# Kernel tuning notes

Measured on AMD Instinct MI355X. Metric: run time of the kernel, lower is better.

## Reference

```python
import jax, jax.numpy as jnp
import numpy as np

DIM = 256
HEADS = 8
HEAD_DIM = 32
INNER = HEADS * HEAD_DIM  # 256
B, L_AG, H, W = 2, 5, 32, 32
SEQ = H * W
POS_HID = 32


def _lin(k, fan_in, fan_out):
    kw, kb = jax.random.split(k)
    Wt = jax.random.normal(kw, (fan_in, fan_out), jnp.float32) * (fan_in ** -0.5)
    b = jax.random.normal(kb, (fan_out,), jnp.float32) * 0.01
    return Wt, b


def setup_inputs() -> dict:
    key = jax.random.key(0)
    ks = jax.random.split(key, 10)
    x = jax.random.normal(ks[0], (B, L_AG, H, W, DIM), jnp.float32)
    Wq, bq = _lin(ks[1], DIM, INNER)
    Wk, bk = _lin(ks[2], DIM, INNER)
    Wv, bv = _lin(ks[3], DIM, INNER)
    Wp1, bp1 = _lin(ks[4], 3, POS_HID)
    Wp2, bp2 = _lin(ks[5], POS_HID, HEADS)
    Ws1, bs1 = _lin(ks[6], DIM, POS_HID)
    Ws2, bs2 = _lin(ks[7], POS_HID, HEADS)
    Wo, bo = _lin(ks[8], INNER, DIM)
    Wg, bg = _lin(ks[9], 2 * DIM, DIM)
    return dict(x=x, Wq=Wq, bq=bq, Wk=Wk, bk=bk, Wv=Wv, bv=bv,
                Wp1=Wp1, bp1=bp1, Wp2=Wp2, bp2=bp2,
                Ws1=Ws1, bs1=bs1, Ws2=Ws2, bs2=bs2,
                Wo=Wo, bo=bo, Wg=Wg, bg=bg)


def _relative_positions(h, w):
    # coords: (h*w, 2), row-major (i//w, i%w) like torch meshgrid 'ij'
    yy, xx = jnp.meshgrid(jnp.arange(h), jnp.arange(w), indexing='ij')
    coords = jnp.stack([yy.reshape(-1), xx.reshape(-1)], axis=-1)  # (L,2)
    rel = (coords[:, None, :] - coords[None, :, :]).astype(jnp.float32)  # (L,L,2)
    dist = jnp.linalg.norm(rel, axis=-1, keepdims=True)  # (L,L,1)
    return jnp.concatenate([rel, dist], axis=-1)  # (L,L,3)


def reference(x, Wq, bq, Wk, bk, Wv, bv, Wp1, bp1, Wp2, bp2,
              Ws1, bs1, Ws2, bs2, Wo, bo, Wg, bg):
    b, l, h, w, c = x.shape
    bl, L = b * l, h * w
    scale = HEAD_DIM ** -0.5
    x2 = x.reshape(bl, L, c)

    q = (x2 @ Wq + bq).reshape(bl, L, HEADS, HEAD_DIM)
    k = (x2 @ Wk + bk).reshape(bl, L, HEADS, HEAD_DIM)
    v = (x2 @ Wv + bv).reshape(bl, L, HEADS, HEAD_DIM)

    scores = jnp.einsum('bihd,bjhd->bhij', q, k) * scale  # (bl,H,L,L)

    rel_pos = _relative_positions(h, w)  # (L,L,3)
    pos_w = jax.nn.relu(rel_pos @ Wp1 + bp1) @ Wp2 + bp2  # (L,L,heads)
    pos_w = jnp.transpose(pos_w, (2, 0, 1))[None]  # (1,heads,L,L)

    s = jax.nn.relu(x2 @ Ws1 + bs1) @ Ws2 + bs2  # (bl,L,heads)
    fsim = jnp.einsum('bih,bjh->bij', s, s)[:, None]  # (bl,1,L,L)

    probs = jax.nn.softmax(scores + pos_w + fsim, axis=-1)
    out = jnp.einsum('bhij,bjhd->bihd', probs, v).reshape(bl, L, INNER)
    out = out @ Wo + bo  # (bl,L,dim); dropout is identity in eval

    gate = jax.nn.sigmoid(jnp.concatenate([x2, out], axis=-1) @ Wg + bg)
    out = gate * out + (1.0 - gate) * x2
    return out.reshape(b, l, h, w, c)
```

## Files before the change

### kernel.cpp

```cpp
#include <hip/hip_runtime.h>

typedef __bf16 bf16_t;
typedef __bf16 bf16x4 __attribute__((ext_vector_type(4)));
typedef __bf16 bf16x8 __attribute__((ext_vector_type(8)));
typedef float  f32x4  __attribute__((ext_vector_type(4)));

#define HEADS 8
#define HEAD_DIM 32
#define DIM 256
#define BL 10
#define SEQ 1024
#define M_TOTAL (BL*SEQ)
#define QK_SCALE 0.17677669529663687f
#define LOG2E 1.4426950408889634f
#define SQRT_LOG2E 1.2011224087864498f
#define NPOS (63*63)

#define NCAST 2596
#define NTRANS 96
#define NPREP (NCAST + NTRANS + 16)

__device__ __forceinline__ int swz_idx(int row, int col) {
  return row*64 + (col ^ ((row & 7) << 3));
}
__device__ __forceinline__ int swz256(int row, int col) {
  return row*256 + (col ^ ((row & 7) << 3));
}

__global__ __launch_bounds__(256) void prep_all_kernel(
    const float* __restrict__ x, const float* __restrict__ Ws1,
    const float* __restrict__ bq, const float* __restrict__ bk,
    const float* __restrict__ bv, const float* __restrict__ bs1,
    const float* __restrict__ Wq, const float* __restrict__ Wk, const float* __restrict__ Wv,
    const float* __restrict__ Wo, const float* __restrict__ Wg,
    const float* __restrict__ Wp1, const float* __restrict__ bp1,
    const float* __restrict__ Wp2, const float* __restrict__ bp2,
    bf16_t* __restrict__ xb, bf16_t* __restrict__ btall, float* __restrict__ bias_all,
    bf16_t* __restrict__ wot, bf16_t* __restrict__ wg1t, bf16_t* __restrict__ wg2t,
    float* __restrict__ posT)
{
  __shared__ float tile[64][65];
  const int bid = blockIdx.x;
  const int tid = threadIdx.x;

  if (bid < NCAST) {
    const int NX4 = M_TOTAL*DIM/4;
    const int i = bid*256 + tid;
    if (i < NX4) {
      const float4 v = ((const float4*)x)[i];
      bf16x4 o; o[0]=(bf16_t)v.x; o[1]=(bf16_t)v.y; o[2]=(bf16_t)v.z; o[3]=(bf16_t)v.w;
      *(bf16x4*)(xb + (size_t)i*4) = o;
      return;
    }
    int idx = i - NX4;
    if (idx < 8192) {
      const int m = idx >> 8, k = idx & 255;
      btall[(768 + m)*256 + k] = (bf16_t)Ws1[k*32 + m];
      return;
    }
    idx -= 8192;
    if (idx < 832) {
      bias_all[idx] = (idx < 256) ? bq[idx] : (idx < 512) ? bk[idx-256] :
                      (idx < 768) ? bv[idx-512] : (idx < 800) ? bs1[idx-768] : 0.f;
    }
    return;
  }

  if (bid < NCAST + NTRANS) {
    const int t0 = bid - NCAST;
    const int z = t0 >> 4, bi = (t0 & 15) >> 2, bj = t0 & 3;
    const float* src; bf16_t* dst;
    switch (z) {
      case 0: src = Wq;          dst = btall;          break;
      case 1: src = Wk;          dst = btall + 65536;  break;
      case 2: src = Wv;          dst = btall + 131072; break;
      case 3: src = Wo;          dst = wot;            break;
      case 4: src = Wg;          dst = wg1t;           break;
      default: src = Wg + 65536; dst = wg2t;           break;
    }
    const int tr = tid >> 4, tc = tid & 15;
    #pragma unroll
    for (int i = 0; i < 4; ++i) {
      const float4 v = *(const float4*)(src + (size_t)(bi*64 + tr + 16*i)*256 + bj*64 + tc*4);
      float* tp = &tile[tr + 16*i][tc*4];
      tp[0]=v.x; tp[1]=v.y; tp[2]=v.z; tp[3]=v.w;
    }
    __syncthreads();
    #pragma unroll
    for (int i = 0; i < 4; ++i) {
      bf16x4 o;
      #pragma unroll
      for (int e = 0; e < 4; ++e) o[e] = (bf16_t)tile[tc*4 + e][tr + 16*i];
      *(bf16x4*)(dst + (size_t)(bj*64 + tr + 16*i)*256 + bi*64 + tc*4) = o;
    }
    return;
  }

  {
    float* sm = &tile[0][0];
    float* w1 = sm; float* b1 = sm + 96; float* w2 = sm + 128; float* b2 = sm + 384;
    if (tid < 96) w1[tid] = Wp1[tid];
    if (tid < 32) b1[tid] = bp1[tid];
    w2[tid] = Wp2[tid];
    if (tid < 8)  b2[tid] = bp2[tid];
    __syncthreads();
    const int p = (bid - NCAST - NTRANS)*256 + tid;
    if (p >= NPOS) return;
    const float dy = (float)(p / 63 - 31);
    const float dx = (float)(p % 63 - 31);
    const float dist = sqrtf(dy*dy + dx*dx);
    float o[8];
    #pragma unroll
    for (int t = 0; t < 8; ++t) o[t] = b2[t];
    #pragma unroll
    for (int m = 0; m < 32; ++m) {
      float hv = fmaf(dy, w1[m], fmaf(dx, w1[32+m], fmaf(dist, w1[64+m], b1[m])));
      hv = fmaxf(hv, 0.f);
      #pragma unroll
      for (int t = 0; t < 8; ++t) o[t] = fmaf(hv, w2[m*8+t], o[t]);
    }
    #pragma unroll
    for (int t = 0; t < 8; ++t) posT[t*NPOS + p] = o[t]*LOG2E;
  }
}

__global__ __launch_bounds__(256) void qkv_kernel(
    const bf16_t* __restrict__ xb, const bf16_t* __restrict__ btall,
    const float* __restrict__ bias_all, const float* __restrict__ Ws2,
    const float* __restrict__ bs2,
    bf16_t* __restrict__ qbuf, bf16_t* __restrict__ kbuf, bf16_t* __restrict__ vbuf,
    bf16_t* __restrict__ sbb)
{
  __shared__ float hidlds[64][33];
  const int mt = blockIdx.x, ngb = blockIdx.y;
  const int tid = threadIdx.x;
  const int w = tid >> 6, lane = tid & 63, g = lane >> 4, l15 = lane & 15;
  const int arow = mt*64 + w*16 + l15;
  const bf16x8* Arow = (const bf16x8*)(xb + (size_t)arow*DIM);
  bf16x8 af[8];
  #pragma unroll
  for (int kc = 0; kc < 8; ++kc) af[kc] = Arow[kc*4 + g];
  if (ngb < 12) {
    bf16_t* dst = (ngb < 4) ? qbuf : (ngb < 8) ? kbuf : vbuf;
    const int coloff = (ngb & 3) * 64;
    const float scale = (ngb < 4) ? QK_SCALE*LOG2E : 1.f;
    for (int c = 0; c < 4; ++c) {
      const int n = ngb*64 + c*16 + l15;
      const bf16x8* Brow = (const bf16x8*)(btall + (size_t)n*DIM);
      f32x4 acc = {0.f,0.f,0.f,0.f};
      #pragma unroll
      for (int kc = 0; kc < 8; ++kc)
        acc = __builtin_amdgcn_mfma_f32_16x16x32_bf16(af[kc], Brow[kc*4+g], acc, 0, 0, 0);
      const float bvv = bias_all[n];
      #pragma unroll
      for (int r = 0; r < 4; ++r) {
        const int row = mt*64 + w*16 + g*4 + r;
        dst[(size_t)row*DIM + coloff + c*16 + l15] = (bf16_t)((acc[r] + bvv)*scale);
      }
    }
  } else {
    for (int c = 0; c < 2; ++c) {
      const int n = 768 + c*16 + l15;
      const bf16x8* Brow = (const bf16x8*)(btall + (size_t)n*DIM);
      f32x4 acc = {0.f,0.f,0.f,0.f};
      #pragma unroll
      for (int kc = 0; kc < 8; ++kc)
        acc = __builtin_amdgcn_mfma_f32_16x16x32_bf16(af[kc], Brow[kc*4+g], acc, 0, 0, 0);
      const float bvv = bias_all[n];
      #pragma unroll
      for (int r = 0; r < 4; ++r)
        hidlds[w*16 + g*4 + r][c*16 + l15] = fmaxf(acc[r] + bvv, 0.f);
    }
    __syncthreads();
    if (tid < 64) {
      float sv[8];
      #pragma unroll
      for (int t = 0; t < 8; ++t) sv[t] = bs2[t];
      #pragma unroll
      for (int m = 0; m < 32; ++m) {
        const float hv = hidlds[tid][m];
        #pragma unroll
        for (int t = 0; t < 8; ++t) sv[t] = fmaf(hv, Ws2[m*8+t], sv[t]);
      }
      bf16x8 o;
      #pragma unroll
      for (int t = 0; t < 8; ++t) o[t] = (bf16_t)(sv[t]*SQRT_LOG2E);
      *(bf16x8*)(sbb + (size_t)(mt*64 + tid)*8) = o;
    }
  }
}

__global__ __launch_bounds__(256) void attn_kernel(
    const bf16_t* __restrict__ qb, const bf16_t* __restrict__ kb,
    const bf16_t* __restrict__ vb, const bf16_t* __restrict__ sbb,
    const float* __restrict__ posT, bf16_t* __restrict__ att)
{
  __shared__ __align__(16) bf16_t lk[64*64];
  __shared__ __align__(16) bf16_t lv[48*64];
  __shared__ __align__(16) bf16_t lp[64*64];
  __shared__ float ptab[33*63];

  const int wg = blockIdx.x;
  const int xcd = wg & 7, within = wg >> 3;
  const int pair = xcd*10 + (within >> 4);
  const int it = within & 15;
  const int h = pair & 7, b = pair >> 3;
  const int i0 = it*64, iy0 = it*2;
  const int tid = threadIdx.x;
  const int w = tid >> 6, lane = tid & 63, g = lane >> 4, l15 = lane & 15;
  const int r4 = tid >> 2, q4 = tid & 3;

  for (int p = tid; p < 33*63; p += 256) {
    const int rr = p / 63, cc = p - rr*63;
    ptab[p] = posT[h*NPOS + (iy0 + rr)*63 + cc];
  }
  for (int p = tid; p < 16*64; p += 256) {
    const int d = 32 + (p >> 6), j = p & 63;
    lv[d*64 + (j ^ ((d & 7) << 3))] = (bf16_t)((d == 32) ? 1.f : 0.f);
  }
  for (int p = tid; p < 192; p += 256) {
    const int rr = p / 3, ch = 5 + (p % 3);
    bf16x8 z = {};
    *(bf16x8*)&lk[swz_idx(rr, ch*8)] = z;
  }

  const int qrow = b*SEQ + i0 + w*16 + l15;
  const bf16x8 aq0 = *(const bf16x8*)(qb + (size_t)qrow*DIM + h*HEAD_DIM + g*8);
  bf16x8 aq1 = {};
  if (g == 0) aq1 = *(const bf16x8*)(sbb + (size_t)qrow*8);

  const int iq = i0 + w*16 + l15;
  const int rbase_i = (iq >> 5) - iy0 + 31;
  const int ixr = iq & 31;

  bf16x8 kreg = *(const bf16x8*)(kb + (size_t)(b*SEQ + r4)*DIM + h*HEAD_DIM + q4*8);
  bf16x8 vreg = *(const bf16x8*)(vb + (size_t)(b*SEQ + r4)*DIM + h*HEAD_DIM + q4*8);
  bf16x8 sreg = {};
  if (tid < 64) sreg = *(const bf16x8*)(sbb + (size_t)(b*SEQ + tid)*8);

  f32x4 accO0 = {0.f,0.f,0.f,0.f}, accO1 = {0.f,0.f,0.f,0.f}, accO2 = {0.f,0.f,0.f,0.f};
  float mrow = -1e30f;

  for (int jt = 0; jt < 16; ++jt) {
    const int j0 = jt*64;
    __syncthreads();
    *(bf16x8*)&lk[swz_idx(r4, q4*8)] = kreg;
    #pragma unroll
    for (int e = 0; e < 8; ++e) {
      const int d = q4*8 + e;
      lv[d*64 + (r4 ^ ((d & 7) << 3))] = vreg[e];
    }
    if (tid < 64) *(bf16x8*)&lk[swz_idx(tid, 32)] = sreg;
    __syncthreads();

    if (jt < 15) {
      const int grow = b*SEQ + j0 + 64;
      kreg = *(const bf16x8*)(kb + (size_t)(grow + r4)*DIM + h*HEAD_DIM + q4*8);
      vreg = *(const bf16x8*)(vb + (size_t)(grow + r4)*DIM + h*HEAD_DIM + q4*8);
      if (tid < 64) sreg = *(const bf16x8*)(sbb + (size_t)(grow + tid)*8);
    }

    f32x4 s4[4];
    #pragma unroll
    for (int c = 0; c < 4; ++c) {
      const bf16x8 kf0 = *(const bf16x8*)&lk[swz_idx(c*16 + l15, g*8)];
      const bf16x8 kf1 = *(const bf16x8*)&lk[swz_idx(c*16 + l15, 32 + g*8)];
      f32x4 acc = {0.f,0.f,0.f,0.f};
      acc = __builtin_amdgcn_mfma_f32_16x16x32_bf16(kf0, aq0, acc, 0, 0, 0);
      acc = __builtin_amdgcn_mfma_f32_16x16x32_bf16(kf1, aq1, acc, 0, 0, 0);
      s4[c] = acc;
    }

    #pragma unroll
    for (int c = 0; c < 4; ++c) {
      #pragma unroll
      for (int r = 0; r < 4; ++r) {
        const int jl = c*16 + g*4 + r;
        const int jy = jt*2 + (jl >> 5);
        const int jx = jl & 31;
        s4[c][r] += ptab[(rbase_i - jy)*63 + (ixr - jx + 31)];
      }
    }

    float m16 = s4[0][0];
    #pragma unroll
    for (int c = 0; c < 4; ++c) {
      #pragma unroll
      for (int r = 0; r < 4; ++r) m16 = fmaxf(m16, s4[c][r]);
    }
    m16 = fmaxf(m16, __shfl_xor(m16, 16));
    m16 = fmaxf(m16, __shfl_xor(m16, 32));
    if (__any(m16 > mrow + 8.f)) {
      const float mn = fmaxf(mrow, m16);
      const float alpha = exp2f(mrow - mn);
      mrow = mn;
      #pragma unroll
      for (int r = 0; r < 4; ++r) {
        const float aO = __shfl(alpha, g*16 + g*4 + r);
        accO0[r] *= aO; accO1[r] *= aO; accO2[r] *= aO;
      }
    }
    #pragma unroll
    for (int c = 0; c < 4; ++c) {
      #pragma unroll
      for (int r = 0; r < 4; ++r) s4[c][r] = exp2f(s4[c][r] - mrow);
    }

    #pragma unroll
    for (int c = 0; c < 4; ++c) {
      bf16x4 o;
      #pragma unroll
      for (int r = 0; r < 4; ++r) o[r] = (bf16_t)s4[c][r];
      *(bf16x4*)&lp[swz_idx(w*16 + l15, c*16 + g*4)] = o;
    }

    const int prow = w*16 + l15;
    #pragma unroll
    for (int kc = 0; kc < 2; ++kc) {
      const bf16x8 ap  = *(const bf16x8*)&lp[swz_idx(prow, kc*32 + g*8)];
      const bf16x8 bv0 = *(const bf16x8*)&lv[swz_idx(l15,      kc*32 + g*8)];
      const bf16x8 bv1 = *(const bf16x8*)&lv[swz_idx(16 + l15, kc*32 + g*8)];
      const bf16x8 bv2 = *(const bf16x8*)&lv[swz_idx(32 + l15, kc*32 + g*8)];
      accO0 = __builtin_amdgcn_mfma_f32_16x16x32_bf16(ap, bv0, accO0, 0, 0, 0);
      accO1 = __builtin_amdgcn_mfma_f32_16x16x32_bf16(ap, bv1, accO1, 0, 0, 0);
      accO2 = __builtin_amdgcn_mfma_f32_16x16x32_bf16(ap, bv2, accO2, 0, 0, 0);
    }
  }

  #pragma unroll
  for (int r = 0; r < 4; ++r) {
    const int row = b*SEQ + i0 + w*16 + g*4 + r;
    const float lsum = __shfl(accO2[r], lane & 48);
    const float inv = 1.f / lsum;
    att[(size_t)row*DIM + h*HEAD_DIM + l15]      = (bf16_t)(accO0[r]*inv);
    att[(size_t)row*DIM + h*HEAD_DIM + 16 + l15] = (bf16_t)(accO1[r]*inv);
  }
}

__global__ __launch_bounds__(256) void prjgate_kernel(
    const bf16_t* __restrict__ att, const bf16_t* __restrict__ wot,
    const float* __restrict__ bo, const bf16_t* __restrict__ xb,
    const float* __restrict__ x, const bf16_t* __restrict__ wg1t,
    const bf16_t* __restrict__ wg2t, const float* __restrict__ bg,
    float* __restrict__ outp)
{
  __shared__ __align__(16) bf16_t prjT[16*256];
  const int row0 = blockIdx.x * 16;
  const int tid = threadIdx.x;
  const int w = tid >> 6, lane = tid & 63, g = lane >> 4, l15 = lane & 15;
  const int arow = row0 + l15;

  {
    const bf16x8* Arow = (const bf16x8*)(att + (size_t)arow*DIM);
    bf16x8 afA[8];
    #pragma unroll
    for (int kc = 0; kc < 8; ++kc) afA[kc] = Arow[kc*4 + g];
    #pragma unroll
    for (int ct = 0; ct < 4; ++ct) {
      const int n = w*64 + ct*16 + l15;
      const bf16x8* Brow = (const bf16x8*)(wot + (size_t)n*DIM);
      f32x4 acc = {0.f,0.f,0.f,0.f};
      #pragma unroll
      for (int kc = 0; kc < 8; ++kc)
        acc = __builtin_amdgcn_mfma_f32_16x16x32_bf16(afA[kc], Brow[kc*4+g], acc, 0, 0, 0);
      const float bvo = bo[n];
      #pragma unroll
      for (int r = 0; r < 4; ++r)
        prjT[swz256(g*4 + r, n)] = (bf16_t)(acc[r] + bvo);
    }
  }
  __syncthreads();

  const bf16x8* A1r = (const bf16x8*)(xb + (size_t)arow*DIM);
  bf16x8 a1[8], a2[8];
  #pragma unroll
  for (int kc = 0; kc < 8; ++kc) {
    a1[kc] = A1r[kc*4 + g];
    a2[kc] = *(const bf16x8*)&prjT[swz256(l15, kc*32 + g*8)];
  }
  #pragma unroll
  for (int ct = 0; ct < 4; ++ct) {
    const int n = w*64 + ct*16 + l15;
    const bf16x8* b1 = (const bf16x8*)(wg1t + (size_t)n*DIM);
    const bf16x8* b2 = (const bf16x8*)(wg2t + (size_t)n*DIM);
    f32x4 acc = {0.f,0.f,0.f,0.f};
    #pragma unroll
    for (int kc = 0; kc < 8; ++kc)
      acc = __builtin_amdgcn_mfma_f32_16x16x32_bf16(a1[kc], b1[kc*4+g], acc, 0, 0, 0);
    #pragma unroll
    for (int kc = 0; kc < 8; ++kc)
      acc = __builtin_amdgcn_mfma_f32_16x16x32_bf16(a2[kc], b2[kc*4+g], acc, 0, 0, 0);
    const float bgv = bg[n];
    #pragma unroll
    for (int r = 0; r < 4; ++r) {
      const int grow = row0 + g*4 + r;
      const float gate = 1.f / (1.f + __expf(-(acc[r] + bgv)));
      const float pv = (float)prjT[swz256(g*4 + r, n)];
      const float xv = x[(size_t)grow*DIM + n];
      outp[(size_t)grow*DIM + n] = gate*pv + (1.f - gate)*xv;
    }
  }
}

extern "C" void kernel_launch(void* const* d_in, const int* in_sizes, int n_in,
                              void* d_out, int out_size, void* d_ws, size_t ws_size,
                              hipStream_t stream)
{
  const float* x   = (const float*)d_in[0];
  const float* Wq  = (const float*)d_in[1];
  const float* bq  = (const float*)d_in[2];
  const float* Wk  = (const float*)d_in[3];
  const float* bk  = (const float*)d_in[4];
  const float* Wv  = (const float*)d_in[5];
  const float* bv  = (const float*)d_in[6];
  const float* Wp1 = (const float*)d_in[7];
  const float* bp1 = (const float*)d_in[8];
  const float* Wp2 = (const float*)d_in[9];
  const float* bp2 = (const float*)d_in[10];
  const float* Ws1 = (const float*)d_in[11];
  const float* bs1 = (const float*)d_in[12];
  const float* Ws2 = (const float*)d_in[13];
  const float* bs2 = (const float*)d_in[14];
  const float* Wo  = (const float*)d_in[15];
  const float* bo  = (const float*)d_in[16];
  const float* Wg  = (const float*)d_in[17];
  const float* bg  = (const float*)d_in[18];

  char* ws = (char*)d_ws;
  size_t off = 0;
  auto alloc = [&](size_t bytes) {
    char* p = ws + off;
    off += (bytes + 255) & ~(size_t)255;
    return p;
  };
  bf16_t* xb    = (bf16_t*)alloc((size_t)M_TOTAL*DIM*2);
  bf16_t* qbuf  = (bf16_t*)alloc((size_t)M_TOTAL*DIM*2);
  bf16_t* kbuf  = (bf16_t*)alloc((size_t)M_TOTAL*DIM*2);
  bf16_t* vbuf  = (bf16_t*)alloc((size_t)M_TOTAL*DIM*2);
  bf16_t* att   = (bf16_t*)alloc((size_t)M_TOTAL*DIM*2);
  bf16_t* btall = (bf16_t*)alloc((size_t)800*256*2);
  bf16_t* wot   = (bf16_t*)alloc(65536*2);
  bf16_t* wg1t  = (bf16_t*)alloc(65536*2);
  bf16_t* wg2t  = (bf16_t*)alloc(65536*2);
  float*  bias_all = (float*)alloc(832*4);
  bf16_t* sbb   = (bf16_t*)alloc((size_t)M_TOTAL*8*2);
  float*  posT  = (float*)alloc((size_t)HEADS*NPOS*4);
  (void)ws_size; (void)in_sizes; (void)n_in; (void)out_size;

  prep_all_kernel<<<NPREP, 256, 0, stream>>>(x, Ws1, bq, bk, bv, bs1,
                                             Wq, Wk, Wv, Wo, Wg, Wp1, bp1, Wp2, bp2,
                                             xb, btall, bias_all, wot, wg1t, wg2t, posT);
  qkv_kernel<<<dim3(M_TOTAL/64, 13), 256, 0, stream>>>(xb, btall, bias_all, Ws2, bs2,
                                                       qbuf, kbuf, vbuf, sbb);
  attn_kernel<<<SEQ/64*HEADS*BL, 256, 0, stream>>>(qbuf, kbuf, vbuf, sbb, posT, att);
  prjgate_kernel<<<M_TOTAL/16, 256, 0, stream>>>(att, wot, bo, xb, x, wg1t, wg2t, bg,
                                                 (float*)d_out);
}
```

Measured before the change: 150.9 us.

## Fuse x bf16 cast into GEMM loads and double query rows per attention block

Drops the separate fp32-to-bf16 pass over x. The QKV and projection/gate kernels now read fp32 x directly and convert in registers. The positional-bias MLP moves from the prep kernel into an extra grid row of the QKV kernel. The attention kernel now handles 128 query rows per block, reusing each loaded K/V tile for two query halves, which halves K/V traffic and the number of blocks at the cost of more registers and a larger ptab.

```diff
diff --git a/kernel.cpp b/kernel.cpp
--- a/kernel.cpp
+++ b/kernel.cpp
@@ -16,9 +16,9 @@
 #define SQRT_LOG2E 1.2011224087864498f
 #define NPOS (63*63)
 
-#define NCAST 2596
+#define NCASTW 36
 #define NTRANS 96
-#define NPREP (NCAST + NTRANS + 16)
+#define NPREP (NCASTW + NTRANS)
 
 __device__ __forceinline__ int swz_idx(int row, int col) {
   return row*64 + (col ^ ((row & 7) << 3));
@@ -28,37 +28,26 @@
 }
 
 __global__ __launch_bounds__(256) void prep_all_kernel(
-    const float* __restrict__ x, const float* __restrict__ Ws1,
+    const float* __restrict__ Ws1,
     const float* __restrict__ bq, const float* __restrict__ bk,
     const float* __restrict__ bv, const float* __restrict__ bs1,
     const float* __restrict__ Wq, const float* __restrict__ Wk, const float* __restrict__ Wv,
     const float* __restrict__ Wo, const float* __restrict__ Wg,
-    const float* __restrict__ Wp1, const float* __restrict__ bp1,
-    const float* __restrict__ Wp2, const float* __restrict__ bp2,
-    bf16_t* __restrict__ xb, bf16_t* __restrict__ btall, float* __restrict__ bias_all,
-    bf16_t* __restrict__ wot, bf16_t* __restrict__ wg1t, bf16_t* __restrict__ wg2t,
-    float* __restrict__ posT)
+    bf16_t* __restrict__ btall, float* __restrict__ bias_all,
+    bf16_t* __restrict__ wot, bf16_t* __restrict__ wg1t, bf16_t* __restrict__ wg2t)
 {
   __shared__ float tile[64][65];
   const int bid = blockIdx.x;
   const int tid = threadIdx.x;
 
-  if (bid < NCAST) {
-    const int NX4 = M_TOTAL*DIM/4;
+  if (bid < NCASTW) {
     const int i = bid*256 + tid;
-    if (i < NX4) {
-      const float4 v = ((const float4*)x)[i];
-      bf16x4 o; o[0]=(bf16_t)v.x; o[1]=(bf16_t)v.y; o[2]=(bf16_t)v.z; o[3]=(bf16_t)v.w;
-      *(bf16x4*)(xb + (size_t)i*4) = o;
-      return;
-    }
-    int idx = i - NX4;
-    if (idx < 8192) {
-      const int m = idx >> 8, k = idx & 255;
+    if (i < 8192) {
+      const int m = i >> 8, k = i & 255;
       btall[(768 + m)*256 + k] = (bf16_t)Ws1[k*32 + m];
       return;
     }
-    idx -= 8192;
+    const int idx = i - 8192;
     if (idx < 832) {
       bias_all[idx] = (idx < 256) ? bq[idx] : (idx < 512) ? bk[idx-256] :
                       (idx < 768) ? bv[idx-512] : (idx < 800) ? bs1[idx-768] : 0.f;
@@ -66,45 +55,56 @@
     return;
   }
 
-  if (bid < NCAST + NTRANS) {
-    const int t0 = bid - NCAST;
-    const int z = t0 >> 4, bi = (t0 & 15) >> 2, bj = t0 & 3;
-    const float* src; bf16_t* dst;
-    switch (z) {
-      case 0: src = Wq;          dst = btall;          break;
-      case 1: src = Wk;          dst = btall + 65536;  break;
-      case 2: src = Wv;          dst = btall + 131072; break;
-      case 3: src = Wo;          dst = wot;            break;
-      case 4: src = Wg;          dst = wg1t;           break;
-      default: src = Wg + 65536; dst = wg2t;           break;
-    }
-    const int tr = tid >> 4, tc = tid & 15;
-    #pragma unroll
-    for (int i = 0; i < 4; ++i) {
-      const float4 v = *(const float4*)(src + (size_t)(bi*64 + tr + 16*i)*256 + bj*64 + tc*4);
-      float* tp = &tile[tr + 16*i][tc*4];
-      tp[0]=v.x; tp[1]=v.y; tp[2]=v.z; tp[3]=v.w;
-    }
-    __syncthreads();
-    #pragma unroll
-    for (int i = 0; i < 4; ++i) {
-      bf16x4 o;
-      #pragma unroll
-      for (int e = 0; e < 4; ++e) o[e] = (bf16_t)tile[tc*4 + e][tr + 16*i];
-      *(bf16x4*)(dst + (size_t)(bj*64 + tr + 16*i)*256 + bi*64 + tc*4) = o;
-    }
-    return;
-  }
-
-  {
-    float* sm = &tile[0][0];
-    float* w1 = sm; float* b1 = sm + 96; float* w2 = sm + 128; float* b2 = sm + 384;
+  const int t0 = bid - NCASTW;
+  const int z = t0 >> 4, bi = (t0 & 15) >> 2, bj = t0 & 3;
+  const float* src; bf16_t* dst;
+  switch (z) {
+    case 0: src = Wq;          dst = btall;          break;
+    case 1: src = Wk;          dst = btall + 65536;  break;
+    case 2: src = Wv;          dst = btall + 131072; break;
+    case 3: src = Wo;          dst = wot;            break;
+    case 4: src = Wg;          dst = wg1t;           break;
+    default: src = Wg + 65536; dst = wg2t;           break;
+  }
+  const int tr = tid >> 4, tc = tid & 15;
+  #pragma unroll
+  for (int i = 0; i < 4; ++i) {
+    const float4 v = *(const float4*)(src + (size_t)(bi*64 + tr + 16*i)*256 + bj*64 + tc*4);
+    float* tp = &tile[tr + 16*i][tc*4];
+    tp[0]=v.x; tp[1]=v.y; tp[2]=v.z; tp[3]=v.w;
+  }
+  __syncthreads();
+  #pragma unroll
+  for (int i = 0; i < 4; ++i) {
+    bf16x4 o;
+    #pragma unroll
+    for (int e = 0; e < 4; ++e) o[e] = (bf16_t)tile[tc*4 + e][tr + 16*i];
+    *(bf16x4*)(dst + (size_t)(bj*64 + tr + 16*i)*256 + bi*64 + tc*4) = o;
+  }
+}
+
+__global__ __launch_bounds__(256) void qkv_kernel(
+    const float* __restrict__ x, const bf16_t* __restrict__ btall,
+    const float* __restrict__ bias_all, const float* __restrict__ Ws2,
+    const float* __restrict__ bs2,
+    const float* __restrict__ Wp1, const float* __restrict__ bp1,
+    const float* __restrict__ Wp2, const float* __restrict__ bp2,
+    bf16_t* __restrict__ qbuf, bf16_t* __restrict__ kbuf, bf16_t* __restrict__ vbuf,
+    bf16_t* __restrict__ sbb, float* __restrict__ posT)
+{
+  __shared__ float smem[64*33];
+  const int mt = blockIdx.x, ngb = blockIdx.y;
+  const int tid = threadIdx.x;
+
+  if (ngb == 13) {
+    if (mt >= 16) return;
+    float* w1 = smem; float* b1 = smem + 96; float* w2 = smem + 128; float* b2 = smem + 384;
     if (tid < 96) w1[tid] = Wp1[tid];
     if (tid < 32) b1[tid] = bp1[tid];
     w2[tid] = Wp2[tid];
     if (tid < 8)  b2[tid] = bp2[tid];
     __syncthreads();
-    const int p = (bid - NCAST - NTRANS)*256 + tid;
+    const int p = mt*256 + tid;
     if (p >= NPOS) return;
     const float dy = (float)(p / 63 - 31);
     const float dx = (float)(p % 63 - 31);
@@ -121,25 +121,21 @@
     }
     #pragma unroll
     for (int t = 0; t < 8; ++t) posT[t*NPOS + p] = o[t]*LOG2E;
-  }
-}
-
-__global__ __launch_bounds__(256) void qkv_kernel(
-    const bf16_t* __restrict__ xb, const bf16_t* __restrict__ btall,
-    const float* __restrict__ bias_all, const float* __restrict__ Ws2,
-    const float* __restrict__ bs2,
-    bf16_t* __restrict__ qbuf, bf16_t* __restrict__ kbuf, bf16_t* __restrict__ vbuf,
-    bf16_t* __restrict__ sbb)
-{
-  __shared__ float hidlds[64][33];
-  const int mt = blockIdx.x, ngb = blockIdx.y;
-  const int tid = threadIdx.x;
+    return;
+  }
+
   const int w = tid >> 6, lane = tid & 63, g = lane >> 4, l15 = lane & 15;
   const int arow = mt*64 + w*16 + l15;
-  const bf16x8* Arow = (const bf16x8*)(xb + (size_t)arow*DIM);
+  const float4* Arow = (const float4*)(x + (size_t)arow*DIM);
   bf16x8 af[8];
   #pragma unroll
-  for (int kc = 0; kc < 8; ++kc) af[kc] = Arow[kc*4 + g];
+  for (int kc = 0; kc < 8; ++kc) {
+    const float4 f0 = Arow[kc*8 + g*2], f1 = Arow[kc*8 + g*2 + 1];
+    bf16x8 v;
+    v[0]=(bf16_t)f0.x; v[1]=(bf16_t)f0.y; v[2]=(bf16_t)f0.z; v[3]=(bf16_t)f0.w;
+    v[4]=(bf16_t)f1.x; v[5]=(bf16_t)f1.y; v[6]=(bf16_t)f1.z; v[7]=(bf16_t)f1.w;
+    af[kc] = v;
+  }
   if (ngb < 12) {
     bf16_t* dst = (ngb < 4) ? qbuf : (ngb < 8) ? kbuf : vbuf;
     const int coloff = (ngb & 3) * 64;
@@ -159,6 +155,7 @@
       }
     }
   } else {
+    float (*hidlds)[33] = (float(*)[33])smem;
     for (int c = 0; c < 2; ++c) {
       const int n = 768 + c*16 + l15;
       const bf16x8* Brow = (const bf16x8*)(btall + (size_t)n*DIM);
@@ -198,19 +195,19 @@
   __shared__ __align__(16) bf16_t lk[64*64];
   __shared__ __align__(16) bf16_t lv[48*64];
   __shared__ __align__(16) bf16_t lp[64*64];
-  __shared__ float ptab[33*63];
+  __shared__ float ptab[35*63];
 
   const int wg = blockIdx.x;
   const int xcd = wg & 7, within = wg >> 3;
-  const int pair = xcd*10 + (within >> 4);
-  const int it = within & 15;
+  const int pair = xcd*10 + (within >> 3);
+  const int it = within & 7;
   const int h = pair & 7, b = pair >> 3;
-  const int i0 = it*64, iy0 = it*2;
+  const int i0 = it*128, iy0 = it*4;
   const int tid = threadIdx.x;
   const int w = tid >> 6, lane = tid & 63, g = lane >> 4, l15 = lane & 15;
   const int r4 = tid >> 2, q4 = tid & 3;
 
-  for (int p = tid; p < 33*63; p += 256) {
+  for (int p = tid; p < 35*63; p += 256) {
     const int rr = p / 63, cc = p - rr*63;
     ptab[p] = posT[h*NPOS + (iy0 + rr)*63 + cc];
   }
@@ -224,22 +221,96 @@
     *(bf16x8*)&lk[swz_idx(rr, ch*8)] = z;
   }
 
-  const int qrow = b*SEQ + i0 + w*16 + l15;
-  const bf16x8 aq0 = *(const bf16x8*)(qb + (size_t)qrow*DIM + h*HEAD_DIM + g*8);
-  bf16x8 aq1 = {};
-  if (g == 0) aq1 = *(const bf16x8*)(sbb + (size_t)qrow*8);
-
-  const int iq = i0 + w*16 + l15;
-  const int rbase_i = (iq >> 5) - iy0 + 31;
-  const int ixr = iq & 31;
+  const int qrowA = b*SEQ + i0 + w*16 + l15;
+  const int qrowB = qrowA + 64;
+  const bf16x8 aq0a = *(const bf16x8*)(qb + (size_t)qrowA*DIM + h*HEAD_DIM + g*8);
+  const bf16x8 aq0b = *(const bf16x8*)(qb + (size_t)qrowB*DIM + h*HEAD_DIM + g*8);
+  bf16x8 aq1a = {}, aq1b = {};
+  if (g == 0) {
+    aq1a = *(const bf16x8*)(sbb + (size_t)qrowA*8);
+    aq1b = *(const bf16x8*)(sbb + (size_t)qrowB*8);
+  }
+
+  const int iqA = i0 + w*16 + l15;
+  const int rbaseA = (iqA >> 5) - iy0 + 31;
+  const int rbaseB = rbaseA + 2;
+  const int ixrA = iqA & 31;
 
   bf16x8 kreg = *(const bf16x8*)(kb + (size_t)(b*SEQ + r4)*DIM + h*HEAD_DIM + q4*8);
   bf16x8 vreg = *(const bf16x8*)(vb + (size_t)(b*SEQ + r4)*DIM + h*HEAD_DIM + q4*8);
   bf16x8 sreg = {};
   if (tid < 64) sreg = *(const bf16x8*)(sbb + (size_t)(b*SEQ + tid)*8);
 
-  f32x4 accO0 = {0.f,0.f,0.f,0.f}, accO1 = {0.f,0.f,0.f,0.f}, accO2 = {0.f,0.f,0.f,0.f};
-  float mrow = -1e30f;
+  f32x4 a0A = {0.f,0.f,0.f,0.f}, a1A = {0.f,0.f,0.f,0.f}, a2A = {0.f,0.f,0.f,0.f};
+  f32x4 a0B = {0.f,0.f,0.f,0.f}, a1B = {0.f,0.f,0.f,0.f}, a2B = {0.f,0.f,0.f,0.f};
+  float mrowA = -1e30f, mrowB = -1e30f;
+
+#define PROCESS_HALF(AQ0, AQ1, RBASE, MROW, A0, A1, A2)                          \
+  {                                                                              \
+    f32x4 s4[4];                                                                 \
+    _Pragma("unroll")                                                            \
+    for (int c = 0; c < 4; ++c) {                                                \
+      const bf16x8 kf0 = *(const bf16x8*)&lk[swz_idx(c*16 + l15, g*8)];          \
+      const bf16x8 kf1 = *(const bf16x8*)&lk[swz_idx(c*16 + l15, 32 + g*8)];     \
+      f32x4 acc = {0.f,0.f,0.f,0.f};                                             \
+      acc = __builtin_amdgcn_mfma_f32_16x16x32_bf16(kf0, AQ0, acc, 0, 0, 0);     \
+      acc = __builtin_amdgcn_mfma_f32_16x16x32_bf16(kf1, AQ1, acc, 0, 0, 0);     \
+      s4[c] = acc;                                                               \
+    }                                                                            \
+    _Pragma("unroll")                                                            \
+    for (int c = 0; c < 4; ++c) {                                                \
+      _Pragma("unroll")                                                          \
+      for (int r = 0; r < 4; ++r) {                                              \
+        const int jl = c*16 + g*4 + r;                                           \
+        const int jy = jt*2 + (jl >> 5);                                         \
+        const int jx = jl & 31;                                                  \
+        s4[c][r] += ptab[((RBASE) - jy)*63 + (ixrA - jx + 31)];                  \
+      }                                                                          \
+    }                                                                            \
+    float m16 = s4[0][0];                                                        \
+    _Pragma("unroll")                                                            \
+    for (int c = 0; c < 4; ++c) {                                                \
+      _Pragma("unroll")                                                          \
+      for (int r = 0; r < 4; ++r) m16 = fmaxf(m16, s4[c][r]);                    \
+    }                                                                            \
+    m16 = fmaxf(m16, __shfl_xor(m16, 16));                                       \
+    m16 = fmaxf(m16, __shfl_xor(m16, 32));                                       \
+    if (__any(m16 > (MROW) + 8.f)) {                                             \
+      const float mn = fmaxf((MROW), m16);                                       \
+      const float alpha = exp2f((MROW) - mn);                                    \
+      (MROW) = mn;                                                               \
+      _Pragma("unroll")                                                          \
+      for (int r = 0; r < 4; ++r) {                                              \
+        const float aO = __shfl(alpha, g*16 + g*4 + r);                          \
+        A0[r] *= aO; A1[r] *= aO; A2[r] *= aO;                                   \
+      }                                                                          \
+    }                                                                            \
+    _Pragma("unroll")                                                            \
+    for (int c = 0; c < 4; ++c) {                                                \
+      _Pragma("unroll")                                                          \
+      for (int r = 0; r < 4; ++r) s4[c][r] = exp2f(s4[c][r] - (MROW));           \
+    }                                                                            \
+    _Pragma("unroll")                                                            \
+    for (int c = 0; c < 4; ++c) {                                                \
+      bf16x4 o;                                                                  \
+      _Pragma("unroll")                                                          \
+      for (int r = 0; r < 4; ++r) o[r] = (bf16_t)s4[c][r];                       \
+      *(bf16x4*)&lp[swz_idx(w*16 + l15, c*16 + g*4)] = o;                        \
+    }                                                                            \
+    {                                                                            \
+      const int prow = w*16 + l15;                                               \
+      _Pragma("unroll")                                                          \
+      for (int kc = 0; kc < 2; ++kc) {                                           \
+        const bf16x8 ap  = *(const bf16x8*)&lp[swz_idx(prow, kc*32 + g*8)];      \
+        const bf16x8 bv0 = *(const bf16x8*)&lv[swz_idx(l15,      kc*32 + g*8)];  \
+        const bf16x8 bv1 = *(const bf16x8*)&lv[swz_idx(16 + l15, kc*32 + g*8)];  \
+        const bf16x8 bv2 = *(const bf16x8*)&lv[swz_idx(32 + l15, kc*32 + g*8)];  \
+        A0 = __builtin_amdgcn_mfma_f32_16x16x32_bf16(ap, bv0, A0, 0, 0, 0);      \
+        A1 = __builtin_amdgcn_mfma_f32_16x16x32_bf16(ap, bv1, A1, 0, 0, 0);      \
+        A2 = __builtin_amdgcn_mfma_f32_16x16x32_bf16(ap, bv2, A2, 0, 0, 0);      \
+      }                                                                          \
+    }                                                                            \
+  }
 
   for (int jt = 0; jt < 16; ++jt) {
     const int j0 = jt*64;
@@ -260,89 +331,29 @@
       if (tid < 64) sreg = *(const bf16x8*)(sbb + (size_t)(grow + tid)*8);
     }
 
-    f32x4 s4[4];
-    #pragma unroll
-    for (int c = 0; c < 4; ++c) {
-      const bf16x8 kf0 = *(const bf16x8*)&lk[swz_idx(c*16 + l15, g*8)];
-      const bf16x8 kf1 = *(const bf16x8*)&lk[swz_idx(c*16 + l15, 32 + g*8)];
-      f32x4 acc = {0.f,0.f,0.f,0.f};
-      acc = __builtin_amdgcn_mfma_f32_16x16x32_bf16(kf0, aq0, acc, 0, 0, 0);
-      acc = __builtin_amdgcn_mfma_f32_16x16x32_bf16(kf1, aq1, acc, 0, 0, 0);
-      s4[c] = acc;
-    }
-
-    #pragma unroll
-    for (int c = 0; c < 4; ++c) {
-      #pragma unroll
-      for (int r = 0; r < 4; ++r) {
-        const int jl = c*16 + g*4 + r;
-        const int jy = jt*2 + (jl >> 5);
-        const int jx = jl & 31;
-        s4[c][r] += ptab[(rbase_i - jy)*63 + (ixr - jx + 31)];
-      }
-    }
-
-    float m16 = s4[0][0];
-    #pragma unroll
-    for (int c = 0; c < 4; ++c) {
-      #pragma unroll
-      for (int r = 0; r < 4; ++r) m16 = fmaxf(m16, s4[c][r]);
-    }
-    m16 = fmaxf(m16, __shfl_xor(m16, 16));
-    m16 = fmaxf(m16, __shfl_xor(m16, 32));
-    if (__any(m16 > mrow + 8.f)) {
-      const float mn = fmaxf(mrow, m16);
-      const float alpha = exp2f(mrow - mn);
-      mrow = mn;
-      #pragma unroll
-      for (int r = 0; r < 4; ++r) {
-        const float aO = __shfl(alpha, g*16 + g*4 + r);
-        accO0[r] *= aO; accO1[r] *= aO; accO2[r] *= aO;
-      }
-    }
-    #pragma unroll
-    for (int c = 0; c < 4; ++c) {
-      #pragma unroll
-      for (int r = 0; r < 4; ++r) s4[c][r] = exp2f(s4[c][r] - mrow);
-    }
-
-    #pragma unroll
-    for (int c = 0; c < 4; ++c) {
-      bf16x4 o;
-      #pragma unroll
-      for (int r = 0; r < 4; ++r) o[r] = (bf16_t)s4[c][r];
-      *(bf16x4*)&lp[swz_idx(w*16 + l15, c*16 + g*4)] = o;
-    }
-
-    const int prow = w*16 + l15;
-    #pragma unroll
-    for (int kc = 0; kc < 2; ++kc) {
-      const bf16x8 ap  = *(const bf16x8*)&lp[swz_idx(prow, kc*32 + g*8)];
-      const bf16x8 bv0 = *(const bf16x8*)&lv[swz_idx(l15,      kc*32 + g*8)];
-      const bf16x8 bv1 = *(const bf16x8*)&lv[swz_idx(16 + l15, kc*32 + g*8)];
-      const bf16x8 bv2 = *(const bf16x8*)&lv[swz_idx(32 + l15, kc*32 + g*8)];
-      accO0 = __builtin_amdgcn_mfma_f32_16x16x32_bf16(ap, bv0, accO0, 0, 0, 0);
-      accO1 = __builtin_amdgcn_mfma_f32_16x16x32_bf16(ap, bv1, accO1, 0, 0, 0);
-      accO2 = __builtin_amdgcn_mfma_f32_16x16x32_bf16(ap, bv2, accO2, 0, 0, 0);
-    }
-  }
+    PROCESS_HALF(aq0a, aq1a, rbaseA, mrowA, a0A, a1A, a2A)
+    PROCESS_HALF(aq0b, aq1b, rbaseB, mrowB, a0B, a1B, a2B)
+  }
+#undef PROCESS_HALF
 
   #pragma unroll
   for (int r = 0; r < 4; ++r) {
-    const int row = b*SEQ + i0 + w*16 + g*4 + r;
-    const float lsum = __shfl(accO2[r], lane & 48);
-    const float inv = 1.f / lsum;
-    att[(size_t)row*DIM + h*HEAD_DIM + l15]      = (bf16_t)(accO0[r]*inv);
-    att[(size_t)row*DIM + h*HEAD_DIM + 16 + l15] = (bf16_t)(accO1[r]*inv);
+    const int rowA = b*SEQ + i0 + w*16 + g*4 + r;
+    const float invA = 1.f / __shfl(a2A[r], lane & 48);
+    att[(size_t)rowA*DIM + h*HEAD_DIM + l15]      = (bf16_t)(a0A[r]*invA);
+    att[(size_t)rowA*DIM + h*HEAD_DIM + 16 + l15] = (bf16_t)(a1A[r]*invA);
+    const int rowB = rowA + 64;
+    const float invB = 1.f / __shfl(a2B[r], lane & 48);
+    att[(size_t)rowB*DIM + h*HEAD_DIM + l15]      = (bf16_t)(a0B[r]*invB);
+    att[(size_t)rowB*DIM + h*HEAD_DIM + 16 + l15] = (bf16_t)(a1B[r]*invB);
   }
 }
 
 __global__ __launch_bounds__(256) void prjgate_kernel(
     const bf16_t* __restrict__ att, const bf16_t* __restrict__ wot,
-    const float* __restrict__ bo, const bf16_t* __restrict__ xb,
-    const float* __restrict__ x, const bf16_t* __restrict__ wg1t,
-    const bf16_t* __restrict__ wg2t, const float* __restrict__ bg,
-    float* __restrict__ outp)
+    const float* __restrict__ bo, const float* __restrict__ x,
+    const bf16_t* __restrict__ wg1t, const bf16_t* __restrict__ wg2t,
+    const float* __restrict__ bg, float* __restrict__ outp)
 {
   __shared__ __align__(16) bf16_t prjT[16*256];
   const int row0 = blockIdx.x * 16;
@@ -371,11 +382,15 @@
   }
   __syncthreads();
 
-  const bf16x8* A1r = (const bf16x8*)(xb + (size_t)arow*DIM);
+  const float4* A1r = (const float4*)(x + (size_t)arow*DIM);
   bf16x8 a1[8], a2[8];
   #pragma unroll
   for (int kc = 0; kc < 8; ++kc) {
-    a1[kc] = A1r[kc*4 + g];
+    const float4 f0 = A1r[kc*8 + g*2], f1 = A1r[kc*8 + g*2 + 1];
+    bf16x8 v;
+    v[0]=(bf16_t)f0.x; v[1]=(bf16_t)f0.y; v[2]=(bf16_t)f0.z; v[3]=(bf16_t)f0.w;
+    v[4]=(bf16_t)f1.x; v[5]=(bf16_t)f1.y; v[6]=(bf16_t)f1.z; v[7]=(bf16_t)f1.w;
+    a1[kc] = v;
     a2[kc] = *(const bf16x8*)&prjT[swz256(l15, kc*32 + g*8)];
   }
   #pragma unroll
@@ -433,7 +448,6 @@
     off += (bytes + 255) & ~(size_t)255;
     return p;
   };
-  bf16_t* xb    = (bf16_t*)alloc((size_t)M_TOTAL*DIM*2);
   bf16_t* qbuf  = (bf16_t*)alloc((size_t)M_TOTAL*DIM*2);
   bf16_t* kbuf  = (bf16_t*)alloc((size_t)M_TOTAL*DIM*2);
   bf16_t* vbuf  = (bf16_t*)alloc((size_t)M_TOTAL*DIM*2);
@@ -447,12 +461,13 @@
   float*  posT  = (float*)alloc((size_t)HEADS*NPOS*4);
   (void)ws_size; (void)in_sizes; (void)n_in; (void)out_size;
 
-  prep_all_kernel<<<NPREP, 256, 0, stream>>>(x, Ws1, bq, bk, bv, bs1,
-                                             Wq, Wk, Wv, Wo, Wg, Wp1, bp1, Wp2, bp2,
-                                             xb, btall, bias_all, wot, wg1t, wg2t, posT);
-  qkv_kernel<<<dim3(M_TOTAL/64, 13), 256, 0, stream>>>(xb, btall, bias_all, Ws2, bs2,
-                                                       qbuf, kbuf, vbuf, sbb);
-  attn_kernel<<<SEQ/64*HEADS*BL, 256, 0, stream>>>(qbuf, kbuf, vbuf, sbb, posT, att);
-  prjgate_kernel<<<M_TOTAL/16, 256, 0, stream>>>(att, wot, bo, xb, x, wg1t, wg2t, bg,
+  prep_all_kernel<<<NPREP, 256, 0, stream>>>(Ws1, bq, bk, bv, bs1,
+                                             Wq, Wk, Wv, Wo, Wg,
+                                             btall, bias_all, wot, wg1t, wg2t);
+  qkv_kernel<<<dim3(M_TOTAL/64, 14), 256, 0, stream>>>(x, btall, bias_all, Ws2, bs2,
+                                                       Wp1, bp1, Wp2, bp2,
+                                                       qbuf, kbuf, vbuf, sbb, posT);
+  attn_kernel<<<SEQ/128*HEADS*BL, 256, 0, stream>>>(qbuf, kbuf, vbuf, sbb, posT, att);
+  prjgate_kernel<<<M_TOTAL/16, 256, 0, stream>>>(att, wot, bo, x, wg1t, wg2t, bg,
                                                  (float*)d_out);
 }
```

Result: slower. 174.7 us (+15.8%).

## Double-buffer K/V tiles in LDS and track softmax row sum in registers

Applied to the files above, without the earlier changes.

The attention loop now ping-pongs two LDS buffers for the K and V tiles. The next tile is written into the spare buffer after the current tile's compute, so each iteration needs one barrier instead of two. The softmax denominator is now summed in fp32 registers and reduced across lanes with shuffles. This removes the ones-column V padding and the third PV MFMA per chunk. LDS use grows for the second buffers, and the row sum now comes from fp32 probabilities rather than their bf16-rounded copies.

```diff
diff --git a/kernel.cpp b/kernel.cpp
--- a/kernel.cpp
+++ b/kernel.cpp
@@ -195,8 +195,8 @@
     const bf16_t* __restrict__ vb, const bf16_t* __restrict__ sbb,
     const float* __restrict__ posT, bf16_t* __restrict__ att)
 {
-  __shared__ __align__(16) bf16_t lk[64*64];
-  __shared__ __align__(16) bf16_t lv[48*64];
+  __shared__ __align__(16) bf16_t lk[2][64*64];
+  __shared__ __align__(16) bf16_t lv[2][32*64];
   __shared__ __align__(16) bf16_t lp[64*64];
   __shared__ float ptab[33*63];
 
@@ -214,14 +214,11 @@
     const int rr = p / 63, cc = p - rr*63;
     ptab[p] = posT[h*NPOS + (iy0 + rr)*63 + cc];
   }
-  for (int p = tid; p < 16*64; p += 256) {
-    const int d = 32 + (p >> 6), j = p & 63;
-    lv[d*64 + (j ^ ((d & 7) << 3))] = (bf16_t)((d == 32) ? 1.f : 0.f);
-  }
-  for (int p = tid; p < 192; p += 256) {
-    const int rr = p / 3, ch = 5 + (p % 3);
+  for (int p = tid; p < 384; p += 256) {
+    const int bufi = p / 192, rem = p - bufi*192;
+    const int rr = rem / 3, ch = 5 + (rem % 3);
     bf16x8 z = {};
-    *(bf16x8*)&lk[swz_idx(rr, ch*8)] = z;
+    *(bf16x8*)&lk[bufi][swz_idx(rr, ch*8)] = z;
   }
 
   const int qrow = b*SEQ + i0 + w*16 + l15;
@@ -237,24 +234,22 @@
   bf16x8 vreg = *(const bf16x8*)(vb + (size_t)(b*SEQ + r4)*DIM + h*HEAD_DIM + q4*8);
   bf16x8 sreg = {};
   if (tid < 64) sreg = *(const bf16x8*)(sbb + (size_t)(b*SEQ + tid)*8);
-
-  f32x4 accO0 = {0.f,0.f,0.f,0.f}, accO1 = {0.f,0.f,0.f,0.f}, accO2 = {0.f,0.f,0.f,0.f};
-  float mrow = -1e30f;
+  *(bf16x8*)&lk[0][swz_idx(r4, q4*8)] = kreg;
+  #pragma unroll
+  for (int e = 0; e < 8; ++e) {
+    const int d = q4*8 + e;
+    lv[0][d*64 + (r4 ^ ((d & 7) << 3))] = vreg[e];
+  }
+  if (tid < 64) *(bf16x8*)&lk[0][swz_idx(tid, 32)] = sreg;
+  __syncthreads();
+
+  f32x4 accO0 = {0.f,0.f,0.f,0.f}, accO1 = {0.f,0.f,0.f,0.f};
+  float mrow = -1e30f, lrow = 0.f;
 
   for (int jt = 0; jt < 16; ++jt) {
-    const int j0 = jt*64;
-    __syncthreads();
-    *(bf16x8*)&lk[swz_idx(r4, q4*8)] = kreg;
-    #pragma unroll
-    for (int e = 0; e < 8; ++e) {
-      const int d = q4*8 + e;
-      lv[d*64 + (r4 ^ ((d & 7) << 3))] = vreg[e];
-    }
-    if (tid < 64) *(bf16x8*)&lk[swz_idx(tid, 32)] = sreg;
-    __syncthreads();
-
+    const int pb = jt & 1;
     if (jt < 15) {
-      const int grow = b*SEQ + j0 + 64;
+      const int grow = b*SEQ + jt*64 + 64;
       kreg = *(const bf16x8*)(kb + (size_t)(grow + r4)*DIM + h*HEAD_DIM + q4*8);
       vreg = *(const bf16x8*)(vb + (size_t)(grow + r4)*DIM + h*HEAD_DIM + q4*8);
       if (tid < 64) sreg = *(const bf16x8*)(sbb + (size_t)(grow + tid)*8);
@@ -263,8 +258,8 @@
     f32x4 s4[4];
     #pragma unroll
     for (int c = 0; c < 4; ++c) {
-      const bf16x8 kf0 = *(const bf16x8*)&lk[swz_idx(c*16 + l15, g*8)];
-      const bf16x8 kf1 = *(const bf16x8*)&lk[swz_idx(c*16 + l15, 32 + g*8)];
+      const bf16x8 kf0 = *(const bf16x8*)&lk[pb][swz_idx(c*16 + l15, g*8)];
+      const bf16x8 kf1 = *(const bf16x8*)&lk[pb][swz_idx(c*16 + l15, 32 + g*8)];
       f32x4 acc = {0.f,0.f,0.f,0.f};
       acc = __builtin_amdgcn_mfma_f32_16x16x32_bf16(kf0, aq0, acc, 0, 0, 0);
       acc = __builtin_amdgcn_mfma_f32_16x16x32_bf16(kf1, aq1, acc, 0, 0, 0);
@@ -294,17 +289,23 @@
       const float mn = fmaxf(mrow, m16);
       const float alpha = exp2f(mrow - mn);
       mrow = mn;
+      lrow *= alpha;
       #pragma unroll
       for (int r = 0; r < 4; ++r) {
         const float aO = __shfl(alpha, g*16 + g*4 + r);
-        accO0[r] *= aO; accO1[r] *= aO; accO2[r] *= aO;
-      }
-    }
-    #pragma unroll
-    for (int c = 0; c < 4; ++c) {
-      #pragma unroll
-      for (int r = 0; r < 4; ++r) s4[c][r] = exp2f(s4[c][r] - mrow);
-    }
+        accO0[r] *= aO; accO1[r] *= aO;
+      }
+    }
+    float rsum = 0.f;
+    #pragma unroll
+    for (int c = 0; c < 4; ++c) {
+      #pragma unroll
+      for (int r = 0; r < 4; ++r) {
+        s4[c][r] = exp2f(s4[c][r] - mrow);
+        rsum += s4[c][r];
+      }
+    }
+    lrow += rsum;
 
     #pragma unroll
     for (int c = 0; c < 4; ++c) {
@@ -318,20 +319,30 @@
     #pragma unroll
     for (int kc = 0; kc < 2; ++kc) {
       const bf16x8 ap  = *(const bf16x8*)&lp[swz_idx(prow, kc*32 + g*8)];
-      const bf16x8 bv0 = *(const bf16x8*)&lv[swz_idx(l15,      kc*32 + g*8)];
-      const bf16x8 bv1 = *(const bf16x8*)&lv[swz_idx(16 + l15, kc*32 + g*8)];
-      const bf16x8 bv2 = *(const bf16x8*)&lv[swz_idx(32 + l15, kc*32 + g*8)];
+      const bf16x8 bv0 = *(const bf16x8*)&lv[pb][swz_idx(l15,      kc*32 + g*8)];
+      const bf16x8 bv1 = *(const bf16x8*)&lv[pb][swz_idx(16 + l15, kc*32 + g*8)];
       accO0 = __builtin_amdgcn_mfma_f32_16x16x32_bf16(ap, bv0, accO0, 0, 0, 0);
       accO1 = __builtin_amdgcn_mfma_f32_16x16x32_bf16(ap, bv1, accO1, 0, 0, 0);
-      accO2 = __builtin_amdgcn_mfma_f32_16x16x32_bf16(ap, bv2, accO2, 0, 0, 0);
-    }
-  }
-
+    }
+
+    if (jt < 15) {
+      *(bf16x8*)&lk[pb^1][swz_idx(r4, q4*8)] = kreg;
+      #pragma unroll
+      for (int e = 0; e < 8; ++e) {
+        const int d = q4*8 + e;
+        lv[pb^1][d*64 + (r4 ^ ((d & 7) << 3))] = vreg[e];
+      }
+      if (tid < 64) *(bf16x8*)&lk[pb^1][swz_idx(tid, 32)] = sreg;
+    }
+    __syncthreads();
+  }
+
+  lrow += __shfl_xor(lrow, 16);
+  lrow += __shfl_xor(lrow, 32);
   #pragma unroll
   for (int r = 0; r < 4; ++r) {
     const int row = b*SEQ + i0 + w*16 + g*4 + r;
-    const float lsum = __shfl(accO2[r], lane & 48);
-    const float inv = 1.f / lsum;
+    const float inv = 1.f / __shfl(lrow, g*16 + g*4 + r);
     att[(size_t)row*DIM + h*HEAD_DIM + l15]      = (bf16_t)(accO0[r]*inv);
     att[(size_t)row*DIM + h*HEAD_DIM + 16 + l15] = (bf16_t)(accO1[r]*inv);
   }
```

Result: faster. 147.2 us (-2.4%).
